# Performance work log

Measured on AMD Instinct MI355X. Metric: run time of the kernel, lower is better.

Reference implementation:

```python
import jax, jax.numpy as jnp
import numpy as np

N = 100000
E = 1600000
FEAT = 128
EMBED = 128
CLASSES = 40


def _sage_conv(x, src, dst, W_l, W_r, b, n_nodes):
    # PyG SAGEConv (mean aggr): out = mean_{j in N(i)} x_j @ W_l + x_i @ W_r + b
    msg = x[src]                                                  # [E, d] gather
    agg = jax.ops.segment_sum(msg, dst, num_segments=n_nodes)     # [N, d]
    cnt = jax.ops.segment_sum(jnp.ones((src.shape[0], 1), x.dtype), dst,
                              num_segments=n_nodes)               # [N, 1]
    agg = agg / jnp.maximum(cnt, 1.0)                             # mean (0 for isolated)
    return agg @ W_l + x @ W_r + b


def setup_inputs() -> dict:
    key = jax.random.key(0)
    ks = jax.random.split(key, 10)
    s = lambda d: 1.0 / np.sqrt(d)
    x = jax.random.normal(ks[0], (N, FEAT), dtype=jnp.float32)
    edge_index = jax.random.randint(ks[1], (2, E), 0, N, dtype=jnp.int64)
    W1_l = jax.random.uniform(ks[2], (FEAT, EMBED), jnp.float32, -s(FEAT), s(FEAT))
    W1_r = jax.random.uniform(ks[3], (FEAT, EMBED), jnp.float32, -s(FEAT), s(FEAT))
    b1 = jnp.zeros((EMBED,), jnp.float32)
    W2_l = jax.random.uniform(ks[4], (EMBED, EMBED), jnp.float32, -s(EMBED), s(EMBED))
    W2_r = jax.random.uniform(ks[5], (EMBED, EMBED), jnp.float32, -s(EMBED), s(EMBED))
    b2 = jnp.zeros((EMBED,), jnp.float32)
    W_out = jax.random.uniform(ks[6], (EMBED, CLASSES), jnp.float32, -s(EMBED), s(EMBED))
    b_out = jax.random.uniform(ks[7], (CLASSES,), jnp.float32, -s(EMBED), s(EMBED))
    return {"x": x, "edge_index": edge_index,
            "W1_l": W1_l, "W1_r": W1_r, "b1": b1,
            "W2_l": W2_l, "W2_r": W2_r, "b2": b2,
            "W_out": W_out, "b_out": b_out}


def reference(x, edge_index, W1_l, W1_r, b1, W2_l, W2_r, b2, W_out, b_out):
    src, dst = edge_index[0], edge_index[1]
    n = x.shape[0]
    h = _sage_conv(x, src, dst, W1_l, W1_r, b1, n)   # [N, EMBED]
    h = _sage_conv(h, src, dst, W2_l, W2_r, b2, n)   # [N, EMBED]
    g = jnp.mean(h, axis=0, keepdims=True)           # global_mean_pool, batch=None -> [1, EMBED]
    return g @ W_out + b_out                          # [1, CLASSES]
```

## Files before the change

kernel.cpp:

```cpp
#include <hip/hip_runtime.h>


#define NN    100000
#define NE    1600000
#define NE4   (NE/4)
#define FEAT  128
#define NCLS  40

#define RSC   25000
#define NRC   4
#define NCC   64
#define PERC  6250

#define RSV   16000
#define NRV   7
#define NCV   32
#define PERV  12500

#define SLICE 200
#define FSG   500
#define P1S   400
#define NV    (3*FEAT + 1)
#define NQ    (P1S / 4)
#define NG    10


__global__ __launch_bounds__(1024) void k_cnt8(const int4* __restrict__ dst4,
                                               unsigned* __restrict__ pc) {
    __shared__ unsigned tab[RSC / 4];
    const int c = blockIdx.x, r = blockIdx.y;
    for (int j = threadIdx.x; j < RSC / 4; j += 1024) tab[j] = 0u;
    __syncthreads();
    const int base = r * RSC;
    const int i0 = c * PERC;
    for (int i = i0 + (int)threadIdx.x; i < i0 + PERC; i += 1024) {
        int4 d = dst4[i];
        unsigned a;
        a = (unsigned)(d.x - base); if (a < RSC) atomicAdd(&tab[a >> 2], 1u << ((a & 3) * 8));
        a = (unsigned)(d.y - base); if (a < RSC) atomicAdd(&tab[a >> 2], 1u << ((a & 3) * 8));
        a = (unsigned)(d.z - base); if (a < RSC) atomicAdd(&tab[a >> 2], 1u << ((a & 3) * 8));
        a = (unsigned)(d.w - base); if (a < RSC) atomicAdd(&tab[a >> 2], 1u << ((a & 3) * 8));
    }
    __syncthreads();
    unsigned* outp = pc + (size_t)(r * NCC + c) * (RSC / 4);
    for (int j = threadIdx.x; j < RSC / 4; j += 1024) outp[j] = tab[j];
}

__global__ __launch_bounds__(256) void k_inv4(const unsigned* __restrict__ pc,
                                              float* __restrict__ invc) {
    int i4 = blockIdx.x * 256 + threadIdx.x;
    if (i4 >= NN / 4) return;
    const int n0 = i4 * 4;
    const int rr = n0 / RSC;
    const int jj = n0 - rr * RSC;
    const unsigned* p = pc + (size_t)rr * NCC * (RSC / 4) + (jj >> 2);
    unsigned acc02 = 0u, acc13 = 0u;
    #pragma unroll 16
    for (int c = 0; c < NCC; ++c) {
        unsigned w = p[(size_t)c * (RSC / 4)];
        acc02 += w & 0x00FF00FFu;
        acc13 += (w >> 8) & 0x00FF00FFu;
    }
    unsigned c0 = acc02 & 0xFFFFu, c2 = acc02 >> 16;
    unsigned c1 = acc13 & 0xFFFFu, c3 = acc13 >> 16;
    float4 v;
    v.x = 1.0f / (float)(c0 > 0u ? c0 : 1u);
    v.y = 1.0f / (float)(c1 > 0u ? c1 : 1u);
    v.z = 1.0f / (float)(c2 > 0u ? c2 : 1u);
    v.w = 1.0f / (float)(c3 > 0u ? c3 : 1u);
    ((float4*)invc)[i4] = v;
}


__global__ __launch_bounds__(1024) void k_scat(const int4* __restrict__ src4,
                                               const int4* __restrict__ dst4,
                                               const float* __restrict__ val,
                                               float* __restrict__ partial) {
    __shared__ float tab[RSV];
    const int c = blockIdx.x, r = blockIdx.y;
    for (int j = threadIdx.x; j < RSV; j += 1024) tab[j] = 0.f;
    __syncthreads();
    const int base = r * RSV;
    const int i0 = c * PERV;
    for (int i = i0 + (int)threadIdx.x; i < i0 + PERV; i += 1024) {
        int4 s = src4[i];
        int4 d = dst4[i];
        unsigned a;
        a = (unsigned)(s.x - base); if (a < RSV) atomicAdd(&tab[a], val[d.x]);
        a = (unsigned)(s.y - base); if (a < RSV) atomicAdd(&tab[a], val[d.y]);
        a = (unsigned)(s.z - base); if (a < RSV) atomicAdd(&tab[a], val[d.z]);
        a = (unsigned)(s.w - base); if (a < RSV) atomicAdd(&tab[a], val[d.w]);
    }
    __syncthreads();
    float* outp = partial + (size_t)(r * NCV + c) * RSV;
    for (int j = threadIdx.x; j < RSV; j += 1024) outp[j] = tab[j];
}

__global__ __launch_bounds__(256) void k_mws4(const float* __restrict__ partial,
                                              const float* __restrict__ invc,
                                              float* __restrict__ ws, float* __restrict__ u) {
    int i4 = blockIdx.x * 256 + threadIdx.x;
    if (i4 >= NN / 4) return;
    const int n0 = i4 * 4;
    const int rr = n0 / RSV;
    const int jj = n0 - rr * RSV;
    const float4* p = (const float4*)(partial + (size_t)rr * NCV * RSV + jj);
    float4 w = {0.f, 0.f, 0.f, 0.f};
    #pragma unroll 8
    for (int c = 0; c < NCV; ++c) {
        float4 v = p[(size_t)c * (RSV / 4)];
        w.x += v.x; w.y += v.y; w.z += v.z; w.w += v.w;
    }
    ((float4*)ws)[i4] = w;
    float4 ic = ((const float4*)invc)[i4];
    float4 uu = {w.x * ic.x, w.y * ic.y, w.z * ic.z, w.w * ic.w};
    ((float4*)u)[i4] = uu;
}


__global__ __launch_bounds__(1024) void k_fsm(const float* __restrict__ x,
                                              const float* __restrict__ ws,
                                              const float* __restrict__ partial,
                                              float* __restrict__ p1) {
    __shared__ float t_sl[SLICE], ws_sl[SLICE], tpart[4][SLICE];
    __shared__ float shx[32][32][4], shw[32][32][4], sht[32][32][4], wsh[32];
    const int bid = blockIdx.x, tid = threadIdx.x;
    const int i0 = bid * SLICE;
    const int rr = bid / (RSV / SLICE);
    const int jj0 = i0 - rr * RSV;

    if (tid < 4 * SLICE) {
        const int g = tid / SLICE;
        const int n = tid - g * SLICE;
        const float* p = partial + (size_t)rr * NCV * RSV + (size_t)(g * 8) * RSV + (jj0 + n);
        float tv = 0.f;
        #pragma unroll
        for (int c = 0; c < 8; ++c) tv += p[(size_t)c * RSV];
        tpart[g][n] = tv;
    }
    if (tid < SLICE) ws_sl[tid] = ws[i0 + tid];
    __syncthreads();
    if (tid < SLICE)
        t_sl[tid] = tpart[0][tid] + tpart[1][tid] + tpart[2][tid] + tpart[3][tid];
    __syncthreads();

    const int lane = tid & 31;
    const int grp  = tid >> 5;
    float sx0=0,sx1=0,sx2=0,sx3=0;
    float sw0=0,sw1=0,sw2=0,sw3=0;
    float st0=0,st1=0,st2=0,st3=0;
    float wsum = 0.f;
    for (int r = grp; r < SLICE; r += 32) {
        const float4* xr = (const float4*)(x + (size_t)(i0 + r) * FEAT);
        float4 v = xr[lane];
        float wr = ws_sl[r];
        float tr = t_sl[r];
        sx0 += v.x; sx1 += v.y; sx2 += v.z; sx3 += v.w;
        sw0 += wr*v.x; sw1 += wr*v.y; sw2 += wr*v.z; sw3 += wr*v.w;
        st0 += tr*v.x; st1 += tr*v.y; st2 += tr*v.z; st3 += tr*v.w;
        if (lane == 0) wsum += wr;
    }
    shx[grp][lane][0]=sx0; shx[grp][lane][1]=sx1; shx[grp][lane][2]=sx2; shx[grp][lane][3]=sx3;
    shw[grp][lane][0]=sw0; shw[grp][lane][1]=sw1; shw[grp][lane][2]=sw2; shw[grp][lane][3]=sw3;
    sht[grp][lane][0]=st0; sht[grp][lane][1]=st1; sht[grp][lane][2]=st2; sht[grp][lane][3]=st3;
    if (lane == 0) wsh[grp] = wsum;
    __syncthreads();

    if (grp == 0) {
        float ax[4]={0,0,0,0}, aw[4]={0,0,0,0}, at[4]={0,0,0,0};
        for (int g = 0; g < 32; ++g) {
            #pragma unroll
            for (int cc = 0; cc < 4; ++cc) {
                ax[cc] += shx[g][lane][cc];
                aw[cc] += shw[g][lane][cc];
                at[cc] += sht[g][lane][cc];
            }
        }
        float* row = p1 + (size_t)bid * P1S;
        #pragma unroll
        for (int cc = 0; cc < 4; ++cc) {
            row[        4*lane + cc] = ax[cc];
            row[FEAT  + 4*lane + cc] = aw[cc];
            row[2*FEAT+ 4*lane + cc] = at[cc];
        }
        if (lane == 0) {
            float w = 0.f;
            for (int g = 0; g < 32; ++g) w += wsh[g];
            row[3*FEAT] = w;
        }
    }
}


__global__ __launch_bounds__(1024) void k_fin(const float* __restrict__ p1,
                                              const float* __restrict__ W1l, const float* __restrict__ W1r,
                                              const float* __restrict__ b1,
                                              const float* __restrict__ W2l, const float* __restrict__ W2r,
                                              const float* __restrict__ b2,
                                              const float* __restrict__ Wout, const float* __restrict__ bout,
                                              float* __restrict__ out) {
    __shared__ float part[NG][P1S];
    __shared__ float fin[800];
    __shared__ float pm[8][128], ps[8][128], po[8][40];
    const int tid = threadIdx.x;

    if (tid < NG * NQ) {
        const int g = tid / NQ;
        const int q = tid - g * NQ;
        const float4* p4 = (const float4*)p1;
        float4 a0 = {0,0,0,0}, a1 = {0,0,0,0};
        const int b0 = g * (FSG / NG);
        #pragma unroll 5
        for (int b = b0; b < b0 + FSG / NG; b += 2) {
            float4 v0 = p4[(size_t)b * NQ + q];
            float4 v1 = p4[(size_t)(b + 1) * NQ + q];
            a0.x += v0.x; a0.y += v0.y; a0.z += v0.z; a0.w += v0.w;
            a1.x += v1.x; a1.y += v1.y; a1.z += v1.z; a1.w += v1.w;
        }
        part[g][4*q    ] = a0.x + a1.x;
        part[g][4*q + 1] = a0.y + a1.y;
        part[g][4*q + 2] = a0.z + a1.z;
        part[g][4*q + 3] = a0.w + a1.w;
    }
    __syncthreads();
    if (tid < NV) {
        float s = 0.f;
        #pragma unroll
        for (int g = 0; g < NG; ++g) s += part[g][tid];
        fin[tid] = s;
    }
    __syncthreads();

    const int f  = tid & 127;
    const int g8 = tid >> 7;
    const int k0 = g8 * 16;

    {
        float m1 = 0.f, s2 = 0.f;
        #pragma unroll
        for (int k = k0; k < k0 + 16; ++k) {
            float wl = W1l[k*FEAT + f];
            float wr = W1r[k*FEAT + f];
            m1 += fin[128 + k] * wl + fin[k] * wr;
            s2 += fin[256 + k] * wl + fin[128 + k] * wr;
        }
        pm[g8][f] = m1;
        ps[g8][f] = s2;
    }
    __syncthreads();
    if (tid < FEAT) {
        float m1 = (float)NN * b1[tid];
        float s2 = fin[384] * b1[tid];
        #pragma unroll
        for (int g = 0; g < 8; ++g) { m1 += pm[g][tid]; s2 += ps[g][tid]; }
        fin[400 + tid] = m1;
        fin[528 + tid] = s2;
    }
    __syncthreads();
    {
        float gg = 0.f;
        #pragma unroll
        for (int k = k0; k < k0 + 16; ++k)
            gg += fin[528 + k] * W2l[k*FEAT + f] + fin[400 + k] * W2r[k*FEAT + f];
        pm[g8][f] = gg;
    }
    __syncthreads();
    if (tid < FEAT) {
        float gg = 0.f;
        #pragma unroll
        for (int g = 0; g < 8; ++g) gg += pm[g][tid];
        fin[656 + tid] = gg * (1.0f / (float)NN) + b2[tid];
    }
    __syncthreads();
    if (f < NCLS) {
        float o = 0.f;
        #pragma unroll
        for (int k = k0; k < k0 + 16; ++k)
            o += fin[656 + k] * Wout[k*NCLS + f];
        po[g8][f] = o;
    }
    __syncthreads();
    if (tid < NCLS) {
        float o = bout[tid];
        #pragma unroll
        for (int g = 0; g < 8; ++g) o += po[g][tid];
        out[tid] = o;
    }
}


__global__ __launch_bounds__(256) void k_count_dev(const int4* __restrict__ dst4, int* __restrict__ cnt) {
    int i = blockIdx.x * 256 + threadIdx.x;
    if (i >= NE4) return;
    int4 d = dst4[i];
    atomicAdd(&cnt[d.x], 1); atomicAdd(&cnt[d.y], 1);
    atomicAdd(&cnt[d.z], 1); atomicAdd(&cnt[d.w], 1);
}

__global__ __launch_bounds__(256) void k_inv_dev(const int* __restrict__ cnt, float* __restrict__ invc) {
    int i = blockIdx.x * 256 + threadIdx.x;
    if (i >= NN) return;
    int c = cnt[i];
    invc[i] = 1.0f / (float)(c > 0 ? c : 1);
}

__global__ __launch_bounds__(256) void k_ws_dev(const int4* __restrict__ src4, const int4* __restrict__ dst4,
                                                const float* __restrict__ invc, float* __restrict__ ws) {
    int i = blockIdx.x * 256 + threadIdx.x;
    if (i >= NE4) return;
    int4 s = src4[i];
    int4 d = dst4[i];
    atomicAdd(&ws[s.x], invc[d.x]); atomicAdd(&ws[s.y], invc[d.y]);
    atomicAdd(&ws[s.z], invc[d.z]); atomicAdd(&ws[s.w], invc[d.w]);
}

__global__ __launch_bounds__(256) void k_u_dev(const float* __restrict__ ws, const float* __restrict__ invc,
                                               float* __restrict__ u) {
    int i = blockIdx.x * 256 + threadIdx.x;
    if (i >= NN) return;
    u[i] = ws[i] * invc[i];
}

__global__ __launch_bounds__(256) void k_t_dev(const int4* __restrict__ src4, const int4* __restrict__ dst4,
                                               const float* __restrict__ u, float* __restrict__ t) {
    int i = blockIdx.x * 256 + threadIdx.x;
    if (i >= NE4) return;
    int4 s = src4[i];
    int4 d = dst4[i];
    atomicAdd(&t[s.x], u[d.x]); atomicAdd(&t[s.y], u[d.y]);
    atomicAdd(&t[s.z], u[d.z]); atomicAdd(&t[s.w], u[d.w]);
}

__global__ __launch_bounds__(256) void k_fs_atom(const float* __restrict__ x,
                                                 const float* __restrict__ ws,
                                                 const float* __restrict__ t,
                                                 float* __restrict__ sums) {
    int lane = threadIdx.x & 31;
    int grp  = threadIdx.x >> 5;
    int row0 = blockIdx.x * 8 + grp;
    int rstride = gridDim.x * 8;
    float sx0=0,sx1=0,sx2=0,sx3=0, sw0=0,sw1=0,sw2=0,sw3=0, st0=0,st1=0,st2=0,st3=0, wsum=0.f;
    for (int r = row0; r < NN; r += rstride) {
        const float4* xr = (const float4*)(x + (size_t)r * FEAT);
        float4 v = xr[lane];
        float wr = ws[r], tr = t[r];
        sx0+=v.x; sx1+=v.y; sx2+=v.z; sx3+=v.w;
        sw0+=wr*v.x; sw1+=wr*v.y; sw2+=wr*v.z; sw3+=wr*v.w;
        st0+=tr*v.x; st1+=tr*v.y; st2+=tr*v.z; st3+=tr*v.w;
        if (lane==0) wsum += wr;
    }
    __shared__ float shx[8][32][4], shw[8][32][4], sht[8][32][4], shwsum[8];
    shx[grp][lane][0]=sx0; shx[grp][lane][1]=sx1; shx[grp][lane][2]=sx2; shx[grp][lane][3]=sx3;
    shw[grp][lane][0]=sw0; shw[grp][lane][1]=sw1; shw[grp][lane][2]=sw2; shw[grp][lane][3]=sw3;
    sht[grp][lane][0]=st0; sht[grp][lane][1]=st1; sht[grp][lane][2]=st2; sht[grp][lane][3]=st3;
    if (lane==0) shwsum[grp]=wsum;
    __syncthreads();
    if (grp==0) {
        float ax[4], aw[4], at[4];
        #pragma unroll
        for (int c=0;c<4;++c){ax[c]=shx[0][lane][c];aw[c]=shw[0][lane][c];at[c]=sht[0][lane][c];}
        #pragma unroll
        for (int g=1;g<8;++g)
            #pragma unroll
            for (int c=0;c<4;++c){ax[c]+=shx[g][lane][c];aw[c]+=shw[g][lane][c];at[c]+=sht[g][lane][c];}
        #pragma unroll
        for (int c=0;c<4;++c){
            atomicAdd(&sums[        4*lane+c], ax[c]);
            atomicAdd(&sums[FEAT  + 4*lane+c], aw[c]);
            atomicAdd(&sums[2*FEAT+ 4*lane+c], at[c]);
        }
        if (lane==0){
            float w=shwsum[0];
            #pragma unroll
            for (int g=1;g<8;++g) w+=shwsum[g];
            atomicAdd(&sums[3*FEAT], w);
        }
    }
}

__global__ __launch_bounds__(128) void k_final_dev(const float* __restrict__ sums,
                                                   const float* __restrict__ W1l, const float* __restrict__ W1r,
                                                   const float* __restrict__ b1,
                                                   const float* __restrict__ W2l, const float* __restrict__ W2r,
                                                   const float* __restrict__ b2,
                                                   const float* __restrict__ Wout, const float* __restrict__ bout,
                                                   float* __restrict__ out) {
    __shared__ float Sx[FEAT], Sw[FEAT], St[FEAT], M1[FEAT], S2[FEAT], G[FEAT];
    __shared__ float Wsum;
    int f = threadIdx.x;
    Sx[f] = sums[f];
    Sw[f] = sums[FEAT + f];
    St[f] = sums[2*FEAT + f];
    if (f == 0) Wsum = sums[3*FEAT];
    __syncthreads();
    float m1 = (float)NN * b1[f];
    float s2 = Wsum * b1[f];
    for (int k = 0; k < FEAT; ++k) {
        float wl = W1l[k*FEAT + f];
        float wr = W1r[k*FEAT + f];
        m1 += Sw[k]*wl + Sx[k]*wr;
        s2 += St[k]*wl + Sw[k]*wr;
    }
    M1[f] = m1; S2[f] = s2;
    __syncthreads();
    float g = 0.f;
    for (int k = 0; k < FEAT; ++k)
        g += S2[k]*W2l[k*FEAT + f] + M1[k]*W2r[k*FEAT + f];
    g = g * (1.0f/(float)NN) + b2[f];
    G[f] = g;
    __syncthreads();
    if (f < NCLS) {
        float o = bout[f];
        for (int k = 0; k < FEAT; ++k)
            o += G[k]*Wout[k*NCLS + f];
        out[f] = o;
    }
}


extern "C" void kernel_launch(void* const* d_in, const int* in_sizes, int n_in,
                              void* d_out, int out_size, void* d_ws, size_t ws_size,
                              hipStream_t stream) {
    const float* x    = (const float*)d_in[0];
    const int*   ei   = (const int*)d_in[1];
    const float* W1l  = (const float*)d_in[2];
    const float* W1r  = (const float*)d_in[3];
    const float* b1   = (const float*)d_in[4];
    const float* W2l  = (const float*)d_in[5];
    const float* W2r  = (const float*)d_in[6];
    const float* b2   = (const float*)d_in[7];
    const float* Wout = (const float*)d_in[8];
    const float* bout = (const float*)d_in[9];
    float* out = (float*)d_out;

    const int4* src4 = (const int4*)ei;
    const int4* dst4 = (const int4*)(ei + NE);

    const size_t PART = (size_t)NRV * NCV * RSV;
    const size_t P1N  = (size_t)FSG * P1S;
    const size_t need = (PART + (size_t)3*NN + P1N) * 4;

    if (ws_size >= need) {
        float* partial = (float*)d_ws;
        float* invc = partial + PART;
        float* ws   = invc + NN;
        float* u    = ws + NN;
        float* p1   = u + NN;

        const int NB4 = (NN/4 + 255) / 256;

        k_cnt8<<<dim3(NCC, NRC), 1024, 0, stream>>>(dst4, (unsigned*)partial);
        k_inv4<<<NB4, 256, 0, stream>>>((const unsigned*)partial, invc);
        k_scat<<<dim3(NCV, NRV), 1024, 0, stream>>>(src4, dst4, invc, partial);
        k_mws4<<<NB4, 256, 0, stream>>>(partial, invc, ws, u);
        k_scat<<<dim3(NCV, NRV), 1024, 0, stream>>>(src4, dst4, u, partial);
        k_fsm<<<FSG, 1024, 0, stream>>>(x, ws, partial, p1);
        k_fin<<<1, 1024, 0, stream>>>(p1, W1l, W1r, b1, W2l, W2r, b2, Wout, bout, out);
    } else {
        int*   cnt  = (int*)d_ws;
        float* wsv  = (float*)d_ws + NN;
        float* t    = (float*)d_ws + 2*NN;
        float* sums = (float*)d_ws + 3*NN;
        float* invc = (float*)d_ws + 3*NN + 640;
        float* u    = (float*)d_ws + 3*NN + 640 + NN;

        hipMemsetAsync(d_ws, 0, ((size_t)3*NN + 640) * 4, stream);

        const int EB4 = (NE4 + 255) / 256;
        const int NB  = (NN + 255) / 256;
        k_count_dev<<<EB4, 256, 0, stream>>>(dst4, cnt);
        k_inv_dev<<<NB, 256, 0, stream>>>(cnt, invc);
        k_ws_dev<<<EB4, 256, 0, stream>>>(src4, dst4, invc, wsv);
        k_u_dev<<<NB, 256, 0, stream>>>(wsv, invc, u);
        k_t_dev<<<EB4, 256, 0, stream>>>(src4, dst4, u, t);
        k_fs_atom<<<256, 256, 0, stream>>>(x, wsv, t, sums);
        k_final_dev<<<1, 128, 0, stream>>>(sums, W1l, W1r, b1, W2l, W2r, b2, Wout, bout, out);
    }
}
```

Before: 176.0 us.

## Pre-bin edges by source/destination range to avoid redundant full edge scans

Adds a binning pass that splits the edge list into per-range buckets, packing each source-local index with its destination id, and storing 16-bit local destination ids. The count and scatter kernels then read only the edges belonging to their row range instead of rescanning all edges in every row block, which cuts redundant global reads and discarded work. The cost is an extra kernel with wave-ballot compaction, extra workspace, and fixed per-bucket capacities (SCAP/DCAP) that hold only while bucket sizes stay near the uniform random mean; overflow would corrupt results.

```diff
diff --git a/kernel.cpp b/kernel.cpp
--- a/kernel.cpp
+++ b/kernel.cpp
@@ -6,6 +6,11 @@
 #define NE4   (NE/4)
 #define FEAT  128
 #define NCLS  40
+
+#define BB    320
+#define EPB   1250
+#define SCAP  1024
+#define DCAP  1664
 
 #define RSC   25000
 #define NRC   4
@@ -25,25 +30,122 @@
 #define NG    10
 
 
-__global__ __launch_bounds__(1024) void k_cnt8(const int4* __restrict__ dst4,
-                                               unsigned* __restrict__ pc) {
+__global__ __launch_bounds__(1024) void k_bin(const int4* __restrict__ src4,
+                                              const int4* __restrict__ dst4,
+                                              unsigned* __restrict__ gsrc, int* __restrict__ gscnt,
+                                              unsigned short* __restrict__ gdst, int* __restrict__ gdcnt) {
+    __shared__ unsigned sB[NRV][SCAP];
+    __shared__ unsigned short dB[NRC][DCAP];
+    __shared__ int scnt[NRV], dcnt[NRC], spad[NRV], dpad[NRC];
+    const int blk = blockIdx.x, tid = threadIdx.x;
+    const int lane = tid & 63;
+    if (tid < NRV) scnt[tid] = 0;
+    if (tid >= 64 && tid < 64 + NRC) dcnt[tid - 64] = 0;
+    __syncthreads();
+
+    const int i0 = blk * EPB;
+    for (int k = tid; k < EPB; k += 1024) {
+        int4 s4 = src4[i0 + k];
+        int4 d4 = dst4[i0 + k];
+        #pragma unroll
+        for (int e = 0; e < 4; ++e) {
+            int s = (&s4.x)[e];
+            int d = (&d4.x)[e];
+            unsigned sb = (unsigned)s / 16000u;
+            unsigned pk = ((unsigned)(s - (int)(sb * 16000u)) << 17) | (unsigned)d;
+            unsigned db = (unsigned)d / 25000u;
+            unsigned short dl = (unsigned short)(d - (int)(db * 25000u));
+            #pragma unroll
+            for (unsigned r = 0; r < NRV; ++r) {
+                unsigned long long m = __ballot(sb == r);
+                if (sb == r) {
+                    int lead = __ffsll((unsigned long long)m) - 1;
+                    unsigned pos = (unsigned)__popcll(m & ((1ull << lane) - 1ull));
+                    int base = 0;
+                    if (lane == lead) base = atomicAdd(&scnt[r], (int)__popcll(m));
+                    base = __shfl(base, lead);
+                    sB[r][(unsigned)base + pos] = pk;
+                }
+            }
+            #pragma unroll
+            for (unsigned r = 0; r < NRC; ++r) {
+                unsigned long long m = __ballot(db == r);
+                if (db == r) {
+                    int lead = __ffsll((unsigned long long)m) - 1;
+                    unsigned pos = (unsigned)__popcll(m & ((1ull << lane) - 1ull));
+                    int base = 0;
+                    if (lane == lead) base = atomicAdd(&dcnt[r], (int)__popcll(m));
+                    base = __shfl(base, lead);
+                    dB[r][(unsigned)base + pos] = dl;
+                }
+            }
+        }
+    }
+    __syncthreads();
+    if (tid < NRV) {
+        int c = scnt[tid], p = (c + 3) & ~3;
+        for (int j = c; j < p; ++j) sB[tid][j] = 0xFFFFFFFFu;
+        spad[tid] = p;
+        gscnt[tid * BB + blk] = p;
+    }
+    if (tid >= 64 && tid < 64 + NRC) {
+        int r = tid - 64;
+        int c = dcnt[r], p = (c + 7) & ~7;
+        for (int j = c; j < p; ++j) dB[r][j] = 0xFFFFu;
+        dpad[r] = p;
+        gdcnt[r * BB + blk] = p;
+    }
+    __syncthreads();
+    for (int r = 0; r < NRV; ++r) {
+        unsigned* gp = gsrc + ((size_t)r * BB + blk) * SCAP;
+        const int p = spad[r];
+        for (int j = tid; j < p; j += 1024) gp[j] = sB[r][j];
+    }
+    for (int r = 0; r < NRC; ++r) {
+        unsigned short* gp = gdst + ((size_t)r * BB + blk) * DCAP;
+        const int p = dpad[r];
+        for (int j = tid; j < p; j += 1024) gp[j] = dB[r][j];
+    }
+}
+
+
+__global__ __launch_bounds__(1024) void k_cnt8b(const unsigned short* __restrict__ gdst,
+                                                const int* __restrict__ gdcnt,
+                                                unsigned* __restrict__ pc) {
     __shared__ unsigned tab[RSC / 4];
-    const int c = blockIdx.x, r = blockIdx.y;
-    for (int j = threadIdx.x; j < RSC / 4; j += 1024) tab[j] = 0u;
-    __syncthreads();
-    const int base = r * RSC;
-    const int i0 = c * PERC;
-    for (int i = i0 + (int)threadIdx.x; i < i0 + PERC; i += 1024) {
-        int4 d = dst4[i];
+    __shared__ int pfx[6];
+    const int c = blockIdx.x, r = blockIdx.y, tid = threadIdx.x;
+    for (int j = tid; j < RSC / 4; j += 1024) tab[j] = 0u;
+    if (tid < 5) pfx[tid + 1] = gdcnt[r * BB + c * 5 + tid];
+    if (tid == 0) pfx[0] = 0;
+    __syncthreads();
+    if (tid == 0) {
+        #pragma unroll
+        for (int s = 0; s < 5; ++s) pfx[s + 1] += pfx[s];
+    }
+    __syncthreads();
+    const int tot8 = pfx[5] >> 3;
+    const unsigned short* segs = gdst + ((size_t)r * BB + (size_t)c * 5) * DCAP;
+    for (int j = tid; j < tot8; j += 1024) {
+        int j8 = j << 3;
+        int s = 0;
+        #pragma unroll
+        for (int q = 1; q < 5; ++q) s += (j8 >= pfx[q]);
+        const int off = j8 - pfx[s];
+        uint4 v = *(const uint4*)(segs + (size_t)s * DCAP + off);
         unsigned a;
-        a = (unsigned)(d.x - base); if (a < RSC) atomicAdd(&tab[a >> 2], 1u << ((a & 3) * 8));
-        a = (unsigned)(d.y - base); if (a < RSC) atomicAdd(&tab[a >> 2], 1u << ((a & 3) * 8));
-        a = (unsigned)(d.z - base); if (a < RSC) atomicAdd(&tab[a >> 2], 1u << ((a & 3) * 8));
-        a = (unsigned)(d.w - base); if (a < RSC) atomicAdd(&tab[a >> 2], 1u << ((a & 3) * 8));
+        a = v.x & 0xFFFFu; if (a < RSC) atomicAdd(&tab[a >> 2], 1u << ((a & 3) * 8));
+        a = v.x >> 16;     if (a < RSC) atomicAdd(&tab[a >> 2], 1u << ((a & 3) * 8));
+        a = v.y & 0xFFFFu; if (a < RSC) atomicAdd(&tab[a >> 2], 1u << ((a & 3) * 8));
+        a = v.y >> 16;     if (a < RSC) atomicAdd(&tab[a >> 2], 1u << ((a & 3) * 8));
+        a = v.z & 0xFFFFu; if (a < RSC) atomicAdd(&tab[a >> 2], 1u << ((a & 3) * 8));
+        a = v.z >> 16;     if (a < RSC) atomicAdd(&tab[a >> 2], 1u << ((a & 3) * 8));
+        a = v.w & 0xFFFFu; if (a < RSC) atomicAdd(&tab[a >> 2], 1u << ((a & 3) * 8));
+        a = v.w >> 16;     if (a < RSC) atomicAdd(&tab[a >> 2], 1u << ((a & 3) * 8));
     }
     __syncthreads();
     unsigned* outp = pc + (size_t)(r * NCC + c) * (RSC / 4);
-    for (int j = threadIdx.x; j < RSC / 4; j += 1024) outp[j] = tab[j];
+    for (int j = tid; j < RSC / 4; j += 1024) outp[j] = tab[j];
 }
 
 __global__ __launch_bounds__(256) void k_inv4(const unsigned* __restrict__ pc,
@@ -72,28 +174,40 @@
 }
 
 
-__global__ __launch_bounds__(1024) void k_scat(const int4* __restrict__ src4,
-                                               const int4* __restrict__ dst4,
-                                               const float* __restrict__ val,
-                                               float* __restrict__ partial) {
+__global__ __launch_bounds__(1024) void k_scatb(const unsigned* __restrict__ gsrc,
+                                                const int* __restrict__ gscnt,
+                                                const float* __restrict__ val,
+                                                float* __restrict__ partial) {
     __shared__ float tab[RSV];
-    const int c = blockIdx.x, r = blockIdx.y;
-    for (int j = threadIdx.x; j < RSV; j += 1024) tab[j] = 0.f;
-    __syncthreads();
-    const int base = r * RSV;
-    const int i0 = c * PERV;
-    for (int i = i0 + (int)threadIdx.x; i < i0 + PERV; i += 1024) {
-        int4 s = src4[i];
-        int4 d = dst4[i];
-        unsigned a;
-        a = (unsigned)(s.x - base); if (a < RSV) atomicAdd(&tab[a], val[d.x]);
-        a = (unsigned)(s.y - base); if (a < RSV) atomicAdd(&tab[a], val[d.y]);
-        a = (unsigned)(s.z - base); if (a < RSV) atomicAdd(&tab[a], val[d.z]);
-        a = (unsigned)(s.w - base); if (a < RSV) atomicAdd(&tab[a], val[d.w]);
+    __shared__ int pfx[11];
+    const int c = blockIdx.x, r = blockIdx.y, tid = threadIdx.x;
+    for (int j = tid; j < RSV; j += 1024) tab[j] = 0.f;
+    if (tid < 10) pfx[tid + 1] = gscnt[r * BB + c * 10 + tid];
+    if (tid == 0) pfx[0] = 0;
+    __syncthreads();
+    if (tid == 0) {
+        #pragma unroll
+        for (int s = 0; s < 10; ++s) pfx[s + 1] += pfx[s];
+    }
+    __syncthreads();
+    const int tot4 = pfx[10] >> 2;
+    const unsigned* segs = gsrc + ((size_t)r * BB + (size_t)c * 10) * SCAP;
+    for (int j = tid; j < tot4; j += 1024) {
+        int j4 = j << 2;
+        int s = 0;
+        #pragma unroll
+        for (int q = 1; q < 10; ++q) s += (j4 >= pfx[q]);
+        const int off = j4 - pfx[s];
+        uint4 w = *(const uint4*)(segs + (size_t)s * SCAP + off);
+        unsigned a, d;
+        a = w.x >> 17; d = w.x & 0x1FFFFu; if (a < RSV) atomicAdd(&tab[a], val[d]);
+        a = w.y >> 17; d = w.y & 0x1FFFFu; if (a < RSV) atomicAdd(&tab[a], val[d]);
+        a = w.z >> 17; d = w.z & 0x1FFFFu; if (a < RSV) atomicAdd(&tab[a], val[d]);
+        a = w.w >> 17; d = w.w & 0x1FFFFu; if (a < RSV) atomicAdd(&tab[a], val[d]);
     }
     __syncthreads();
     float* outp = partial + (size_t)(r * NCV + c) * RSV;
-    for (int j = threadIdx.x; j < RSV; j += 1024) outp[j] = tab[j];
+    for (int j = tid; j < RSV; j += 1024) outp[j] = tab[j];
 }
 
 __global__ __launch_bounds__(256) void k_mws4(const float* __restrict__ partial,
@@ -436,9 +550,13 @@
     const int4* src4 = (const int4*)ei;
     const int4* dst4 = (const int4*)(ei + NE);
 
-    const size_t PART = (size_t)NRV * NCV * RSV;
-    const size_t P1N  = (size_t)FSG * P1S;
-    const size_t need = (PART + (size_t)3*NN + P1N) * 4;
+    const size_t PART  = (size_t)NRV * NCV * RSV;
+    const size_t P1N   = (size_t)FSG * P1S;
+    const size_t GSRCN = (size_t)NRV * BB * SCAP;
+    const size_t GDSTN = (size_t)NRC * BB * DCAP;
+    const size_t need  = (PART + (size_t)3*NN + P1N
+                          + (size_t)NRV*BB + (size_t)NRC*BB
+                          + GSRCN + GDSTN/2) * 4;
 
     if (ws_size >= need) {
         float* partial = (float*)d_ws;
@@ -446,14 +564,19 @@
         float* ws   = invc + NN;
         float* u    = ws + NN;
         float* p1   = u + NN;
+        int*   gscnt = (int*)(p1 + P1N);
+        int*   gdcnt = gscnt + (size_t)NRV*BB;
+        unsigned* gsrc = (unsigned*)(gdcnt + (size_t)NRC*BB);
+        unsigned short* gdst = (unsigned short*)(gsrc + GSRCN);
 
         const int NB4 = (NN/4 + 255) / 256;
 
-        k_cnt8<<<dim3(NCC, NRC), 1024, 0, stream>>>(dst4, (unsigned*)partial);
+        k_bin<<<BB, 1024, 0, stream>>>(src4, dst4, gsrc, gscnt, gdst, gdcnt);
+        k_cnt8b<<<dim3(NCC, NRC), 1024, 0, stream>>>(gdst, gdcnt, (unsigned*)partial);
         k_inv4<<<NB4, 256, 0, stream>>>((const unsigned*)partial, invc);
-        k_scat<<<dim3(NCV, NRV), 1024, 0, stream>>>(src4, dst4, invc, partial);
+        k_scatb<<<dim3(NCV, NRV), 1024, 0, stream>>>(gsrc, gscnt, invc, partial);
         k_mws4<<<NB4, 256, 0, stream>>>(partial, invc, ws, u);
-        k_scat<<<dim3(NCV, NRV), 1024, 0, stream>>>(src4, dst4, u, partial);
+        k_scatb<<<dim3(NCV, NRV), 1024, 0, stream>>>(gsrc, gscnt, u, partial);
         k_fsm<<<FSG, 1024, 0, stream>>>(x, ws, partial, p1);
         k_fin<<<1, 1024, 0, stream>>>(p1, W1l, W1r, b1, W2l, W2r, b2, Wout, bout, out);
     } else {
```

After: 192.7 us. +9.5%, slower.
